# Optimization experiments

Measured on AMD Instinct MI355X. Metric: run time of the kernel, lower is better.

The kernel has to match this reference:

```python
import jax, jax.numpy as jnp
import numpy as np

TEMPERATURE = 0.05
EPS = 1e-12  # F.normalize eps


def _l2norm(x):
    n = jnp.sqrt(jnp.sum(x * x, axis=-1, keepdims=True))
    return x / jnp.maximum(n, EPS)


def setup_inputs() -> dict:
    key = jax.random.key(0)
    k1, k2, k3 = jax.random.split(key, 3)
    B, S, D = 8, 1536, 1024
    h1 = jax.random.normal(k1, (B, S, D), dtype=jnp.float32)
    h2 = jax.random.normal(k2, (B, S, D), dtype=jnp.float32)
    mask = jax.random.randint(k3, (B, S), 0, 2).astype(bool)
    return {"last_hidden_states_1": h1, "last_hidden_states_2": h2, "token_mask_batch": mask}


def reference(last_hidden_states_1, last_hidden_states_2, token_mask_batch):
    # Vectorized equivalent of the per-sample python loop: padded (masked) tokens
    # simply contribute nothing to pos/neg sums or the mean.
    B, S, D = last_hidden_states_1.shape
    f1 = _l2norm(last_hidden_states_1)  # [B,S,D]
    f2 = _l2norm(last_hidden_states_2)
    feats = jnp.concatenate([f1, f2], axis=1)  # [B,2S,D]

    # positive pairs: token i in view1 vs token i in view2
    pos_sim = jnp.sum(f1 * f2, axis=-1).astype(jnp.float32) / TEMPERATURE  # [B,S]
    pos = jnp.exp(jnp.concatenate([pos_sim, pos_sim], axis=1))  # [B,2S]

    # all-pairs similarities among the 2n effective tokens
    sim = jnp.einsum("bid,bjd->bij", feats, feats).astype(jnp.float32) / TEMPERATURE  # [B,2S,2S]

    m2 = jnp.concatenate([token_mask_batch, token_mask_batch], axis=1)  # [B,2S]
    tok = jnp.arange(2 * S) % S
    same_token = tok[:, None] == tok[None, :]  # excludes self and its positive counterpart
    neg_mask = m2[:, :, None] & m2[:, None, :] & (~same_token)  # [B,2S,2S]

    Ng = jnp.sum(jnp.exp(sim) * neg_mask, axis=-1)  # [B,2S]
    per_tok = -jnp.log(pos / (Ng + pos))  # [B,2S]

    m2f = m2.astype(jnp.float32)
    per_sample = jnp.sum(per_tok * m2f, axis=1) / jnp.sum(m2f, axis=1)  # mean over 2n tokens
    return jnp.mean(per_sample)
```

## Files before the change

### kernel.cpp

```cpp
#include <hip/hip_runtime.h>
#include <hip/hip_bf16.h>
#include <math.h>

#define BATCH 8
#define SEQ   1536
#define DIM   1024
#define SEQ2  (2*SEQ)
#define TEMP_INV 20.0f
#define EXP_SCALE (TEMP_INV / 64.0f)

#define BM 128
#define BN 128
#define BK 128
#define KITERS (DIM/BK)
#define TILES  (SEQ2 / BM)
#define NPAIRS (TILES * (TILES+1) / 2)

typedef int   i32x4 __attribute__((ext_vector_type(4)));
typedef int   i32x8 __attribute__((ext_vector_type(8)));
typedef float f32x4 __attribute__((ext_vector_type(4)));

#define GLOBAL_AS __attribute__((address_space(1)))
#define LDS_AS    __attribute__((address_space(3)))

__device__ inline void async_ld16(const void* g, void* lds_uniform) {
    __builtin_amdgcn_global_load_lds((const GLOBAL_AS void*)g, (LDS_AS void*)lds_uniform, 16, 0, 0);
}

__device__ inline float wave_red64(float v) {
    #pragma unroll
    for (int m = 32; m > 0; m >>= 1) v += __shfl_xor(v, m, 64);
    return v;
}

__global__ __launch_bounds__(256) void normalize_kernel(
        const float* __restrict__ h1, const float* __restrict__ h2,
        unsigned char* __restrict__ feats, float* __restrict__ pos_cos,
        float* __restrict__ Ng, float* __restrict__ out) {
    int w = threadIdx.x >> 6, lane = threadIdx.x & 63;
    int tok = blockIdx.x * 4 + w;
    int b = tok / SEQ, s = tok - b * SEQ;

    const float4* a4 = (const float4*)(h1 + (size_t)tok * DIM);
    const float4* b4 = (const float4*)(h2 + (size_t)tok * DIM);
    float4 av[4], bv[4];
    #pragma unroll
    for (int it = 0; it < 4; it++) { av[it] = a4[lane + 64*it]; bv[it] = b4[lane + 64*it]; }

    float ss1 = 0.f, ss2 = 0.f, sd = 0.f;
    #pragma unroll
    for (int it = 0; it < 4; it++) {
        ss1 += av[it].x*av[it].x + av[it].y*av[it].y + av[it].z*av[it].z + av[it].w*av[it].w;
        ss2 += bv[it].x*bv[it].x + bv[it].y*bv[it].y + bv[it].z*bv[it].z + bv[it].w*bv[it].w;
        sd  += av[it].x*bv[it].x + av[it].y*bv[it].y + av[it].z*bv[it].z + av[it].w*bv[it].w;
    }
    ss1 = wave_red64(ss1); ss2 = wave_red64(ss2); sd = wave_red64(sd);

    float sc1 = 1.0f / fmaxf(sqrtf(ss1), 1e-12f);
    float sc2 = 1.0f / fmaxf(sqrtf(ss2), 1e-12f);
    float s18 = sc1 * 8.0f, s28 = sc2 * 8.0f;

    unsigned int* f1row = (unsigned int*)(feats + ((size_t)b * SEQ2 + s) * DIM);
    unsigned int* f2row = (unsigned int*)(feats + ((size_t)b * SEQ2 + SEQ + s) * DIM);
    #pragma unroll
    for (int it = 0; it < 4; it++) {
        int p1 = __builtin_amdgcn_cvt_pk_fp8_f32(av[it].x * s18, av[it].y * s18, 0, 0);
        p1     = __builtin_amdgcn_cvt_pk_fp8_f32(av[it].z * s18, av[it].w * s18, p1, 1);
        int p2 = __builtin_amdgcn_cvt_pk_fp8_f32(bv[it].x * s28, bv[it].y * s28, 0, 0);
        p2     = __builtin_amdgcn_cvt_pk_fp8_f32(bv[it].z * s28, bv[it].w * s28, p2, 1);
        f1row[lane + 64*it] = (unsigned int)p1;
        f2row[lane + 64*it] = (unsigned int)p2;
    }
    if (lane == 0) {
        pos_cos[tok] = sd * sc1 * sc2;
        Ng[2*tok] = 0.0f;
        Ng[2*tok + 1] = 0.0f;
        if (tok == 0) out[0] = 0.0f;
    }
}

__global__ __launch_bounds__(256) void gemm_ng_kernel(
        const unsigned char* __restrict__ feats, const int* __restrict__ mask,
        float* __restrict__ Ng) {
    int bid = blockIdx.x;
    int b = bid & 7;
    int p = bid >> 3;
    int ti = 0;
    while (p >= TILES - ti) { p -= TILES - ti; ti++; }
    int tj = ti + p;
    int ibase = ti * BM, jbase = tj * BN;
    bool isdiag = (ti == tj);

    const unsigned char* fb = feats + (size_t)b * SEQ2 * DIM;

    __shared__ __align__(16) unsigned char As[2][BM][BK];
    __shared__ __align__(16) unsigned char Bs[2][BN][BK];
    __shared__ float mrow_s[BM];
    __shared__ float mcol_s[BN];

    int t = threadIdx.x;
    int lane = t & 63, w = t >> 6;
    int wrow = w >> 1, wcol = w & 1;
    int colq = lane & 15, quad = lane >> 4;

    int sr = t >> 3;
    int sc = (t & 7) ^ (sr & 7);
    const unsigned char* a0 = fb + (size_t)(ibase + sr) * DIM + sc * 16;
    const unsigned char* b0 = fb + (size_t)(jbase + sr) * DIM + sc * 16;

    auto stage = [&](int it, int buf) {
        size_t kb = (size_t)it * BK;
        #pragma unroll
        for (int q = 0; q < 4; q++) {
            async_ld16(a0 + (size_t)q * 32 * DIM + kb, (char*)&As[buf][0][0] + q * 4096 + w * 1024);
            async_ld16(b0 + (size_t)q * 32 * DIM + kb, (char*)&Bs[buf][0][0] + q * 4096 + w * 1024);
        }
    };

    stage(0, 0);

    if (t < BM) {
        int i = ibase + t; int im = (i < SEQ) ? i : i - SEQ;
        mrow_s[t] = mask[b * SEQ + im] ? 1.0f : 0.0f;
    } else {
        int j = jbase + (t - BM); int jm = (j < SEQ) ? j : j - SEQ;
        mcol_s[t - BM] = mask[b * SEQ + jm] ? 1.0f : 0.0f;
    }

    f32x4 acc[4][4] = {};
    int s0 = ((2 * quad)     ^ (colq & 7)) * 16;
    int s1 = ((2 * quad + 1) ^ (colq & 7)) * 16;

    int buf = 0;
    #pragma unroll 1
    for (int it = 0; it < KITERS; it++) {
        __syncthreads();

        i32x8 af[4], bg[4];
        #pragma unroll
        for (int mi = 0; mi < 4; mi++) {
            int row = wrow * 64 + mi * 16 + colq;
            i32x4 lo = *(const i32x4*)&As[buf][row][s0];
            i32x4 hi = *(const i32x4*)&As[buf][row][s1];
            af[mi] = __builtin_shufflevector(lo, hi, 0, 1, 2, 3, 4, 5, 6, 7);
        }
        #pragma unroll
        for (int nj = 0; nj < 4; nj++) {
            int row = wcol * 64 + nj * 16 + colq;
            i32x4 lo = *(const i32x4*)&Bs[buf][row][s0];
            i32x4 hi = *(const i32x4*)&Bs[buf][row][s1];
            bg[nj] = __builtin_shufflevector(lo, hi, 0, 1, 2, 3, 4, 5, 6, 7);
        }

        if (it + 1 < KITERS) stage(it + 1, buf ^ 1);

        #pragma unroll
        for (int mi = 0; mi < 4; mi++)
            #pragma unroll
            for (int nj = 0; nj < 4; nj++)
                acc[mi][nj] = __builtin_amdgcn_mfma_scale_f32_16x16x128_f8f6f4(
                    af[mi], bg[nj], acc[mi][nj],
                    0, 0,
                    0, 0x7F7F7F7F,
                    0, 0x7F7F7F7F);
        buf ^= 1;
    }

    float mj[4]; int jglob[4];
    #pragma unroll
    for (int nj = 0; nj < 4; nj++) {
        int jl = wcol * 64 + nj * 16 + colq;
        mj[nj] = mcol_s[jl];
        jglob[nj] = jbase + jl;
    }
    float colsum[4] = {0.f, 0.f, 0.f, 0.f};

    #pragma unroll
    for (int mi = 0; mi < 4; mi++) {
        int il0 = wrow * 64 + mi * 16 + quad * 4;
        float rsum[4] = {0.f, 0.f, 0.f, 0.f};
        float mr[4];
        #pragma unroll
        for (int r = 0; r < 4; r++) mr[r] = mrow_s[il0 + r];
        #pragma unroll
        for (int nj = 0; nj < 4; nj++) {
            #pragma unroll
            for (int r = 0; r < 4; r++) {
                int d = (ibase + il0 + r) - jglob[nj];
                bool same = (d == 0) | (d == SEQ) | (d == -SEQ);
                float e = same ? 0.0f : __expf(acc[mi][nj][r] * EXP_SCALE);
                rsum[r] += e * mj[nj];
                colsum[nj] += e * mr[r];
            }
        }
        #pragma unroll
        for (int r = 0; r < 4; r++) {
            float v = rsum[r];
            #pragma unroll
            for (int m = 1; m < 16; m <<= 1) v += __shfl_xor(v, m, 64);
            if (colq == 0)
                atomicAdd(&Ng[b * SEQ2 + ibase + il0 + r], v);
        }
    }

    if (!isdiag) {
        #pragma unroll
        for (int nj = 0; nj < 4; nj++) {
            float v = colsum[nj];
            v += __shfl_xor(v, 16, 64);
            v += __shfl_xor(v, 32, 64);
            if (quad == 0)
                atomicAdd(&Ng[b * SEQ2 + jglob[nj]], v);
        }
    }
}

__global__ __launch_bounds__(256) void loss_kernel(
        const float* __restrict__ Ng, const float* __restrict__ pos_cos,
        const int* __restrict__ mask, float* __restrict__ out) {
    int b = blockIdx.x, t = threadIdx.x;
    float sum = 0.f, cnt = 0.f;
    for (int i = t; i < SEQ2; i += 256) {
        int im = (i < SEQ) ? i : i - SEQ;
        if (mask[b * SEQ + im]) {
            float ps = pos_cos[b * SEQ + im] * TEMP_INV;
            float ng = Ng[b * SEQ2 + i];
            sum += log1pf(ng * __expf(-ps));
            cnt += 1.0f;
        }
    }
    sum = wave_red64(sum); cnt = wave_red64(cnt);
    __shared__ float rs[4], rc[4];
    int lane = t & 63, w = t >> 6;
    if (lane == 0) { rs[w] = sum; rc[w] = cnt; }
    __syncthreads();
    if (t == 0) {
        float s = rs[0]+rs[1]+rs[2]+rs[3];
        float c = rc[0]+rc[1]+rc[2]+rc[3];
        atomicAdd(out, s / c * (1.0f / BATCH));
    }
}

extern "C" void kernel_launch(void* const* d_in, const int* in_sizes, int n_in,
                              void* d_out, int out_size, void* d_ws, size_t ws_size,
                              hipStream_t stream) {
    const float* h1  = (const float*)d_in[0];
    const float* h2  = (const float*)d_in[1];
    const int* mask  = (const int*)d_in[2];
    float* out       = (float*)d_out;

    char* ws = (char*)d_ws;
    size_t feats_bytes = (size_t)BATCH * SEQ2 * DIM;
    unsigned char* feats = (unsigned char*)ws;
    float* pos_cos    = (float*)(ws + feats_bytes);
    float* Ng         = (float*)(ws + feats_bytes + (size_t)BATCH * SEQ * 4);

    normalize_kernel<<<BATCH * SEQ / 4, 256, 0, stream>>>(h1, h2, feats, pos_cos, Ng, out);

    gemm_ng_kernel<<<NPAIRS * BATCH, 256, 0, stream>>>(feats, mask, Ng);

    loss_kernel<<<BATCH, 256, 0, stream>>>(Ng, pos_cos, mask, out);
}
```

Before: 206.9 us.

## Enlarge GEMM tiles to 256x256 with 8-wave phased ping-pong MFMA schedule

The fp8 similarity GEMM now uses 256x256 output tiles computed by 512 threads (2x4 waves), each wave holding 8x4 MFMA accumulators. Each K-tile is split into halves that are loaded asynchronously and interleaved with MFMA phases, using explicit barriers, lgkm/vm waitcnts and s_setprio. This is meant to raise operand reuse and overlap global-to-LDS loads with matrix math. It also cuts the block count, which risks load imbalance across CUs, and the larger tile raises register pressure. The loss kernel is widened to 1024 threads.

```diff
diff --git a/kernel.cpp b/kernel.cpp
--- a/kernel.cpp
+++ b/kernel.cpp
@@ -9,10 +9,11 @@
 #define TEMP_INV 20.0f
 #define EXP_SCALE (TEMP_INV / 64.0f)
 
-#define BM 128
-#define BN 128
+#define BM 256
+#define BN 256
 #define BK 128
-#define KITERS (DIM/BK)
+#define KTILES (DIM/BK)
+#define GITERS (KTILES/2)
 #define TILES  (SEQ2 / BM)
 #define NPAIRS (TILES * (TILES+1) / 2)
 
@@ -79,7 +80,7 @@
     }
 }
 
-__global__ __launch_bounds__(256) void gemm_ng_kernel(
+__global__ __launch_bounds__(512, 2) void gemm_ng_kernel(
         const unsigned char* __restrict__ feats, const int* __restrict__ mask,
         float* __restrict__ Ng) {
     int bid = blockIdx.x;
@@ -93,31 +94,36 @@
 
     const unsigned char* fb = feats + (size_t)b * SEQ2 * DIM;
 
-    __shared__ __align__(16) unsigned char As[2][BM][BK];
-    __shared__ __align__(16) unsigned char Bs[2][BN][BK];
+    __shared__ __align__(16) unsigned char As[2][2][128][BK];
+    __shared__ __align__(16) unsigned char Bs[2][2][128][BK];
     __shared__ float mrow_s[BM];
     __shared__ float mcol_s[BN];
 
     int t = threadIdx.x;
     int lane = t & 63, w = t >> 6;
-    int wrow = w >> 1, wcol = w & 1;
+    int wrow = w >> 2, wcol = w & 3;
     int colq = lane & 15, quad = lane >> 4;
 
-    int sr = t >> 3;
-    int sc = (t & 7) ^ (sr & 7);
-    const unsigned char* a0 = fb + (size_t)(ibase + sr) * DIM + sc * 16;
-    const unsigned char* b0 = fb + (size_t)(jbase + sr) * DIM + sc * 16;
-
-    auto stage = [&](int it, int buf) {
-        size_t kb = (size_t)it * BK;
-        #pragma unroll
-        for (int q = 0; q < 4; q++) {
-            async_ld16(a0 + (size_t)q * 32 * DIM + kb, (char*)&As[buf][0][0] + q * 4096 + w * 1024);
-            async_ld16(b0 + (size_t)q * 32 * DIM + kb, (char*)&Bs[buf][0][0] + q * 4096 + w * 1024);
-        }
-    };
-
-    stage(0, 0);
+    int sr8 = lane >> 3;
+    int sc  = (lane & 7) ^ sr8;
+    const unsigned char* aSrc = fb + (size_t)(ibase + w*16 + sr8) * DIM + sc*16;
+    const unsigned char* bSrc = fb + (size_t)(jbase + w*16 + sr8) * DIM + sc*16;
+
+    auto stA = [&](int kt, int h) {
+        char* lb = (char*)&As[kt & 1][h][0][0] + w * 2048;
+        const unsigned char* g = aSrc + (size_t)(h * 128) * DIM + (size_t)kt * BK;
+        async_ld16(g,               lb);
+        async_ld16(g + 8 * DIM,     lb + 1024);
+    };
+    auto stB = [&](int kt, int h) {
+        char* lb = (char*)&Bs[kt & 1][h][0][0] + w * 2048;
+        const unsigned char* g = bSrc + (size_t)(h * 128) * DIM + (size_t)kt * BK;
+        async_ld16(g,               lb);
+        async_ld16(g + 8 * DIM,     lb + 1024);
+    };
+
+    stA(0, 0); stA(0, 1); stB(0, 0); stB(0, 1);
+    stA(1, 0);
 
     if (t < BM) {
         int i = ibase + t; int im = (i < SEQ) ? i : i - SEQ;
@@ -126,44 +132,101 @@
         int j = jbase + (t - BM); int jm = (j < SEQ) ? j : j - SEQ;
         mcol_s[t - BM] = mask[b * SEQ + jm] ? 1.0f : 0.0f;
     }
-
-    f32x4 acc[4][4] = {};
-    int s0 = ((2 * quad)     ^ (colq & 7)) * 16;
-    int s1 = ((2 * quad + 1) ^ (colq & 7)) * 16;
-
-    int buf = 0;
-    #pragma unroll 1
-    for (int it = 0; it < KITERS; it++) {
-        __syncthreads();
-
-        i32x8 af[4], bg[4];
-        #pragma unroll
-        for (int mi = 0; mi < 4; mi++) {
-            int row = wrow * 64 + mi * 16 + colq;
-            i32x4 lo = *(const i32x4*)&As[buf][row][s0];
-            i32x4 hi = *(const i32x4*)&As[buf][row][s1];
-            af[mi] = __builtin_shufflevector(lo, hi, 0, 1, 2, 3, 4, 5, 6, 7);
-        }
-        #pragma unroll
-        for (int nj = 0; nj < 4; nj++) {
-            int row = wcol * 64 + nj * 16 + colq;
-            i32x4 lo = *(const i32x4*)&Bs[buf][row][s0];
-            i32x4 hi = *(const i32x4*)&Bs[buf][row][s1];
-            bg[nj] = __builtin_shufflevector(lo, hi, 0, 1, 2, 3, 4, 5, 6, 7);
-        }
-
-        if (it + 1 < KITERS) stage(it + 1, buf ^ 1);
-
-        #pragma unroll
-        for (int mi = 0; mi < 4; mi++)
+    __syncthreads();
+
+    int as0 = ((2 * quad)     ^ (colq & 7)) * 16;
+    int as1 = ((2 * quad + 1) ^ (colq & 7)) * 16;
+
+    auto rdA = [&](int d, int mi) -> i32x8 {
+        const unsigned char* row = &As[d][wrow][mi * 16 + colq][0];
+        i32x4 lo = *(const i32x4*)(row + as0);
+        i32x4 hi = *(const i32x4*)(row + as1);
+        return __builtin_shufflevector(lo, hi, 0, 1, 2, 3, 4, 5, 6, 7);
+    };
+    auto rdB = [&](int d, int nj) -> i32x8 {
+        int J = wcol * 64 + nj * 16 + colq;
+        const unsigned char* row = &Bs[d][J >> 7][J & 127][0];
+        i32x4 lo = *(const i32x4*)(row + as0);
+        i32x4 hi = *(const i32x4*)(row + as1);
+        return __builtin_shufflevector(lo, hi, 0, 1, 2, 3, 4, 5, 6, 7);
+    };
+
+    f32x4 acc[8][4] = {};
+
+    auto MQ = [&](i32x8* a, i32x8* bq, int mg, int ng) {
+        #pragma unroll
+        for (int x = 0; x < 4; x++)
             #pragma unroll
-            for (int nj = 0; nj < 4; nj++)
-                acc[mi][nj] = __builtin_amdgcn_mfma_scale_f32_16x16x128_f8f6f4(
-                    af[mi], bg[nj], acc[mi][nj],
+            for (int y = 0; y < 2; y++)
+                acc[mg*4 + x][ng*2 + y] = __builtin_amdgcn_mfma_scale_f32_16x16x128_f8f6f4(
+                    a[x], bq[y], acc[mg*4 + x][ng*2 + y],
                     0, 0,
                     0, 0x7F7F7F7F,
                     0, 0x7F7F7F7F);
-        buf ^= 1;
+    };
+
+    #define PH_BAR()  __builtin_amdgcn_s_barrier()
+    #define PH_LGKM() asm volatile("s_waitcnt lgkmcnt(0)" ::: "memory")
+
+    i32x8 a[4], b01[2], b23[2];
+
+    #pragma unroll
+    for (int i = 0; i < GITERS; i++) {
+        const int k1 = 2*i + 1;
+        const bool more = (i < GITERS - 1);
+
+        #pragma unroll
+        for (int x = 0; x < 4; x++) a[x] = rdA(0, x);
+        b01[0] = rdB(0, 0); b01[1] = rdB(0, 1);
+        stA(k1, 1);
+        PH_BAR(); PH_LGKM();
+        __builtin_amdgcn_s_setprio(1); MQ(a, b01, 0, 0); __builtin_amdgcn_s_setprio(0);
+        PH_BAR();
+        b23[0] = rdB(0, 2); b23[1] = rdB(0, 3);
+        stB(k1, 0);
+        PH_BAR(); PH_LGKM();
+        __builtin_amdgcn_s_setprio(1); MQ(a, b23, 0, 1); __builtin_amdgcn_s_setprio(0);
+        PH_BAR();
+        #pragma unroll
+        for (int x = 0; x < 4; x++) a[x] = rdA(0, 4 + x);
+        stB(k1, 1);
+        PH_BAR(); PH_LGKM();
+        __builtin_amdgcn_s_setprio(1); MQ(a, b23, 1, 1); __builtin_amdgcn_s_setprio(0);
+        PH_BAR();
+        if (more) {
+            stA(2*i + 2, 0);
+            asm volatile("s_waitcnt vmcnt(2)" ::: "memory");
+        } else {
+            asm volatile("s_waitcnt vmcnt(0)" ::: "memory");
+        }
+        PH_BAR();
+        __builtin_amdgcn_s_setprio(1); MQ(a, b01, 1, 0); __builtin_amdgcn_s_setprio(0);
+        PH_BAR();
+        #pragma unroll
+        for (int x = 0; x < 4; x++) a[x] = rdA(1, x);
+        b01[0] = rdB(1, 0); b01[1] = rdB(1, 1);
+        if (more) stA(2*i + 2, 1);
+        PH_BAR(); PH_LGKM();
+        __builtin_amdgcn_s_setprio(1); MQ(a, b01, 0, 0); __builtin_amdgcn_s_setprio(0);
+        PH_BAR();
+        b23[0] = rdB(1, 2); b23[1] = rdB(1, 3);
+        if (more) stB(2*i + 2, 0);
+        PH_BAR(); PH_LGKM();
+        __builtin_amdgcn_s_setprio(1); MQ(a, b23, 0, 1); __builtin_amdgcn_s_setprio(0);
+        PH_BAR();
+        #pragma unroll
+        for (int x = 0; x < 4; x++) a[x] = rdA(1, 4 + x);
+        if (more) stB(2*i + 2, 1);
+        PH_BAR(); PH_LGKM();
+        __builtin_amdgcn_s_setprio(1); MQ(a, b23, 1, 1); __builtin_amdgcn_s_setprio(0);
+        PH_BAR();
+        if (more) {
+            stA(2*i + 3, 0);
+            asm volatile("s_waitcnt vmcnt(2)" ::: "memory");
+        }
+        PH_BAR();
+        __builtin_amdgcn_s_setprio(1); MQ(a, b01, 1, 0); __builtin_amdgcn_s_setprio(0);
+        PH_BAR();
     }
 
     float mj[4]; int jglob[4];
@@ -176,8 +239,8 @@
     float colsum[4] = {0.f, 0.f, 0.f, 0.f};
 
     #pragma unroll
-    for (int mi = 0; mi < 4; mi++) {
-        int il0 = wrow * 64 + mi * 16 + quad * 4;
+    for (int mi = 0; mi < 8; mi++) {
+        int il0 = wrow * 128 + mi * 16 + quad * 4;
         float rsum[4] = {0.f, 0.f, 0.f, 0.f};
         float mr[4];
         #pragma unroll
@@ -215,12 +278,12 @@
     }
 }
 
-__global__ __launch_bounds__(256) void loss_kernel(
+__global__ __launch_bounds__(1024) void loss_kernel(
         const float* __restrict__ Ng, const float* __restrict__ pos_cos,
         const int* __restrict__ mask, float* __restrict__ out) {
     int b = blockIdx.x, t = threadIdx.x;
     float sum = 0.f, cnt = 0.f;
-    for (int i = t; i < SEQ2; i += 256) {
+    for (int i = t; i < SEQ2; i += 1024) {
         int im = (i < SEQ) ? i : i - SEQ;
         if (mask[b * SEQ + im]) {
             float ps = pos_cos[b * SEQ + im] * TEMP_INV;
@@ -230,13 +293,14 @@
         }
     }
     sum = wave_red64(sum); cnt = wave_red64(cnt);
-    __shared__ float rs[4], rc[4];
+    __shared__ float rs[16], rc[16];
     int lane = t & 63, w = t >> 6;
     if (lane == 0) { rs[w] = sum; rc[w] = cnt; }
     __syncthreads();
     if (t == 0) {
-        float s = rs[0]+rs[1]+rs[2]+rs[3];
-        float c = rc[0]+rc[1]+rc[2]+rc[3];
+        float s = 0.f, c = 0.f;
+        #pragma unroll
+        for (int k = 0; k < 16; k++) { s += rs[k]; c += rc[k]; }
         atomicAdd(out, s / c * (1.0f / BATCH));
     }
 }
@@ -257,7 +321,7 @@
 
     normalize_kernel<<<BATCH * SEQ / 4, 256, 0, stream>>>(h1, h2, feats, pos_cos, Ng, out);
 
-    gemm_ng_kernel<<<NPAIRS * BATCH, 256, 0, stream>>>(feats, mask, Ng);
-
-    loss_kernel<<<BATCH, 256, 0, stream>>>(Ng, pos_cos, mask, out);
-}
+    gemm_ng_kernel<<<NPAIRS * BATCH, 512, 0, stream>>>(feats, mask, Ng);
+
+    loss_kernel<<<BATCH, 1024, 0, stream>>>(Ng, pos_cos, mask, out);
+}
```

Result: slower. 246.3 us (+19.0%).

## Single-buffer GEMM LDS tiles for higher occupancy and widen loss reduction

Applied to the files above, without the earlier changes.

Drops the double-buffered LDS staging in the fp8 similarity GEMM to a single buffer, halving LDS per block to about 32KB, and requests 3 blocks per CU via launch bounds. Global-to-LDS prefetch of the next K slice now starts after fragments are read into registers and a barrier, then overlaps with the MFMA work, with an extra barrier per iteration. The aim is to hide latency through more resident blocks rather than in-block double buffering, at the cost of more synchronisation and possible register pressure. The loss kernel is also widened to 1024 threads per block.

```diff
diff --git a/kernel.cpp b/kernel.cpp
--- a/kernel.cpp
+++ b/kernel.cpp
@@ -79,7 +79,7 @@
     }
 }
 
-__global__ __launch_bounds__(256) void gemm_ng_kernel(
+__global__ __launch_bounds__(256, 3) void gemm_ng_kernel(
         const unsigned char* __restrict__ feats, const int* __restrict__ mask,
         float* __restrict__ Ng) {
     int bid = blockIdx.x;
@@ -93,8 +93,8 @@
 
     const unsigned char* fb = feats + (size_t)b * SEQ2 * DIM;
 
-    __shared__ __align__(16) unsigned char As[2][BM][BK];
-    __shared__ __align__(16) unsigned char Bs[2][BN][BK];
+    __shared__ __align__(16) unsigned char As[BM][BK];
+    __shared__ __align__(16) unsigned char Bs[BN][BK];
     __shared__ float mrow_s[BM];
     __shared__ float mcol_s[BN];
 
@@ -108,16 +108,16 @@
     const unsigned char* a0 = fb + (size_t)(ibase + sr) * DIM + sc * 16;
     const unsigned char* b0 = fb + (size_t)(jbase + sr) * DIM + sc * 16;
 
-    auto stage = [&](int it, int buf) {
+    auto stage = [&](int it) {
         size_t kb = (size_t)it * BK;
         #pragma unroll
         for (int q = 0; q < 4; q++) {
-            async_ld16(a0 + (size_t)q * 32 * DIM + kb, (char*)&As[buf][0][0] + q * 4096 + w * 1024);
-            async_ld16(b0 + (size_t)q * 32 * DIM + kb, (char*)&Bs[buf][0][0] + q * 4096 + w * 1024);
+            async_ld16(a0 + (size_t)q * 32 * DIM + kb, (char*)&As[0][0] + q * 4096 + w * 1024);
+            async_ld16(b0 + (size_t)q * 32 * DIM + kb, (char*)&Bs[0][0] + q * 4096 + w * 1024);
         }
     };
 
-    stage(0, 0);
+    stage(0);
 
     if (t < BM) {
         int i = ibase + t; int im = (i < SEQ) ? i : i - SEQ;
@@ -126,33 +126,36 @@
         int j = jbase + (t - BM); int jm = (j < SEQ) ? j : j - SEQ;
         mcol_s[t - BM] = mask[b * SEQ + jm] ? 1.0f : 0.0f;
     }
+    __syncthreads();
 
     f32x4 acc[4][4] = {};
     int s0 = ((2 * quad)     ^ (colq & 7)) * 16;
     int s1 = ((2 * quad + 1) ^ (colq & 7)) * 16;
 
-    int buf = 0;
     #pragma unroll 1
     for (int it = 0; it < KITERS; it++) {
-        __syncthreads();
-
         i32x8 af[4], bg[4];
         #pragma unroll
         for (int mi = 0; mi < 4; mi++) {
             int row = wrow * 64 + mi * 16 + colq;
-            i32x4 lo = *(const i32x4*)&As[buf][row][s0];
-            i32x4 hi = *(const i32x4*)&As[buf][row][s1];
+            i32x4 lo = *(const i32x4*)&As[row][s0];
+            i32x4 hi = *(const i32x4*)&As[row][s1];
             af[mi] = __builtin_shufflevector(lo, hi, 0, 1, 2, 3, 4, 5, 6, 7);
         }
         #pragma unroll
         for (int nj = 0; nj < 4; nj++) {
             int row = wcol * 64 + nj * 16 + colq;
-            i32x4 lo = *(const i32x4*)&Bs[buf][row][s0];
-            i32x4 hi = *(const i32x4*)&Bs[buf][row][s1];
+            i32x4 lo = *(const i32x4*)&Bs[row][s0];
+            i32x4 hi = *(const i32x4*)&Bs[row][s1];
             bg[nj] = __builtin_shufflevector(lo, hi, 0, 1, 2, 3, 4, 5, 6, 7);
         }
 
-        if (it + 1 < KITERS) stage(it + 1, buf ^ 1);
+        __syncthreads();
+
+        if (it + 1 < KITERS) {
+            stage(it + 1);
+            __builtin_amdgcn_sched_barrier(0);
+        }
 
         #pragma unroll
         for (int mi = 0; mi < 4; mi++)
@@ -163,7 +166,9 @@
                     0, 0,
                     0, 0x7F7F7F7F,
                     0, 0x7F7F7F7F);
-        buf ^= 1;
+
+        if (it + 1 < KITERS)
+            __syncthreads();
     }
 
     float mj[4]; int jglob[4];
@@ -215,12 +220,12 @@
     }
 }
 
-__global__ __launch_bounds__(256) void loss_kernel(
+__global__ __launch_bounds__(1024) void loss_kernel(
         const float* __restrict__ Ng, const float* __restrict__ pos_cos,
         const int* __restrict__ mask, float* __restrict__ out) {
     int b = blockIdx.x, t = threadIdx.x;
     float sum = 0.f, cnt = 0.f;
-    for (int i = t; i < SEQ2; i += 256) {
+    for (int i = t; i < SEQ2; i += 1024) {
         int im = (i < SEQ) ? i : i - SEQ;
         if (mask[b * SEQ + im]) {
             float ps = pos_cos[b * SEQ + im] * TEMP_INV;
@@ -230,13 +235,14 @@
         }
     }
     sum = wave_red64(sum); cnt = wave_red64(cnt);
-    __shared__ float rs[4], rc[4];
+    __shared__ float rs[16], rc[16];
     int lane = t & 63, w = t >> 6;
     if (lane == 0) { rs[w] = sum; rc[w] = cnt; }
     __syncthreads();
     if (t == 0) {
-        float s = rs[0]+rs[1]+rs[2]+rs[3];
-        float c = rc[0]+rc[1]+rc[2]+rc[3];
+        float s = 0.f, c = 0.f;
+        #pragma unroll
+        for (int k = 0; k < 16; k++) { s += rs[k]; c += rc[k]; }
         atomicAdd(out, s / c * (1.0f / BATCH));
     }
 }
@@ -259,5 +265,5 @@
 
     gemm_ng_kernel<<<NPAIRS * BATCH, 256, 0, stream>>>(feats, mask, Ng);
 
-    loss_kernel<<<BATCH, 256, 0, stream>>>(Ng, pos_cos, mask, out);
-}
+    loss_kernel<<<BATCH, 1024, 0, stream>>>(Ng, pos_cos, mask, out);
+}
```

After: 193.6 us. 1.07x faster.
